# Optimization experiments

Measured on AMD Instinct MI355X. Metric: run time of the kernel, lower is better.

Reference implementation:

```python
import jax, jax.numpy as jnp
import numpy as np

B, S, D, H, L, MLP, WIN = 4, 1024, 256, 8, 2, 1024, 64
HD = D // H
NEG = -1e9  # emulates -inf additive mask; exp underflows to exact 0

_idx = jnp.arange(S)
BAND = jnp.where(jnp.abs(_idx[:, None] - _idx[None, :]) <= WIN, 0.0, NEG).astype(jnp.float32)


def setup_inputs() -> dict:
    key = jax.random.key(0)
    ks = iter(jax.random.split(key, 16))
    r = lambda shape, s=0.02: jax.random.normal(next(ks), shape, dtype=jnp.float32) * s
    return {
        "x": jax.random.normal(next(ks), (B, S, D), dtype=jnp.float32),
        "scale": jnp.ones((1,), jnp.float32) * (D ** -0.5),
        "Win_a": r((L, 3 * D, D)), "bin_a": jnp.zeros((L, 3 * D), jnp.float32),
        "Wout_a": r((L, D, D)), "bout_a": jnp.zeros((L, D), jnp.float32),
        "Win_e": r((L, 3 * D, D)), "bin_e": jnp.zeros((L, 3 * D), jnp.float32),
        "Wout_e": r((L, D, D)), "bout_e": jnp.zeros((L, D), jnp.float32),
        "ln1_g": jnp.ones((L, D), jnp.float32), "ln1_b": jnp.zeros((L, D), jnp.float32),
        "ln2_g": jnp.ones((L, D), jnp.float32), "ln2_b": jnp.zeros((L, D), jnp.float32),
        "W1": r((L, MLP, D)), "b1": jnp.zeros((L, MLP), jnp.float32),
        "W2": r((L, D, MLP)), "b2": jnp.zeros((L, D), jnp.float32),
        "lnf_g": jnp.ones((D,), jnp.float32), "lnf_b": jnp.zeros((D,), jnp.float32),
    }


def _layernorm(x, g, b, eps=1e-5):
    m = jnp.mean(x, axis=-1, keepdims=True)
    v = jnp.mean(jnp.square(x - m), axis=-1, keepdims=True)
    return (x - m) * jax.lax.rsqrt(v + eps) * g + b


def _mha(x, Win, bin_, Wout, bout, mask=None):
    # torch nn.MultiheadAttention (batch_first=True), dropout=0
    b, s, _ = x.shape
    qkv = x @ Win.T + bin_                       # (b, s, 3D)
    q, k, v = jnp.split(qkv, 3, axis=-1)
    split = lambda t: t.reshape(b, s, H, HD).transpose(0, 2, 1, 3)  # (b, H, s, HD)
    q, k, v = split(q), split(k), split(v)
    scores = jnp.einsum('bhqd,bhkd->bhqk', q, k) / np.float32(np.sqrt(HD))
    if mask is not None:
        scores = scores + mask
    attn = jax.nn.softmax(scores, axis=-1)
    out = jnp.einsum('bhqk,bhkd->bhqd', attn, v).transpose(0, 2, 1, 3).reshape(b, s, D)
    return out @ Wout.T + bout


def reference(x, scale, Win_a, bin_a, Wout_a, bout_a, Win_e, bin_e, Wout_e, bout_e,
              ln1_g, ln1_b, ln2_g, ln2_b, W1, b1, W2, b2, lnf_g, lnf_b):
    # ScaledSinusoidalPositionalEncoding returns arange(S)*scale, shape (S,1)
    pos = jnp.arange(S, dtype=jnp.float32) * scale[0]   # (S,)
    x = x + pos[:, None]                                 # broadcast (B,S,D)+(S,1)
    for l in range(L):
        xi = _mha(x, Win_a[l], bin_a[l], Wout_a[l], bout_a[l])
        x = _layernorm(x + xi, ln1_g[l], ln1_b[l])
        xe = _mha(x, Win_e[l], bin_e[l], Wout_e[l], bout_e[l], mask=BAND)
        attended = _layernorm(x + xe, ln2_g[l], ln2_b[l])
        h = jax.nn.gelu(attended @ W1[l].T + b1[l], approximate=False)
        x = attended + h @ W2[l].T + b2[l]
    return _layernorm(x, lnf_g, lnf_b)
```

## Files before the change

kernel.cpp:

```cpp
#include <hip/hip_runtime.h>
#include <math.h>

#define BB 4
#define SS 1024
#define DD 256
#define HH 8
#define HD 32
#define D3 768
#define MLP 1024
#define NTOK (BB * SS)
#define NSEG 4

typedef __attribute__((ext_vector_type(8))) short short8;
typedef __attribute__((ext_vector_type(4))) float f32x4;

__device__ __forceinline__ unsigned short f2bfu(float f) {
    union { float f; unsigned i; } u; u.f = f;
    unsigned r = u.i + 0x7fffu + ((u.i >> 16) & 1u);
    return (unsigned short)(r >> 16);
}
__device__ __forceinline__ float bfu2f(unsigned short h) {
    union { unsigned i; float f; } u; u.i = ((unsigned)h) << 16; return u.f;
}

#define W_TOT 2097152
#define WL0   196608
#define WBLK  (W_TOT / 256)
#define PBLK  (NTOK * DD / 256)
__global__ __launch_bounds__(256) void prep_kernel(
    const float* __restrict__ a0, const float* __restrict__ a1,
    const float* __restrict__ a2, const float* __restrict__ a3,
    const float* __restrict__ a4, const float* __restrict__ a5,
    unsigned short* __restrict__ out, unsigned short* __restrict__ out_lo,
    const float* __restrict__ x, const float* __restrict__ scale,
    float* __restrict__ xf, unsigned short* __restrict__ xh,
    unsigned short* __restrict__ xl)
{
    if (blockIdx.x < WBLK) {
        int i = blockIdx.x * 256 + threadIdx.x;
        const float* s; int off;
        if      (i <  393216) { s = a0; off = 0;       }
        else if (i <  524288) { s = a1; off = 393216;  }
        else if (i <  917504) { s = a2; off = 524288;  }
        else if (i < 1048576) { s = a3; off = 917504;  }
        else if (i < 1572864) { s = a4; off = 1048576; }
        else                  { s = a5; off = 1572864; }
        float v = s[i - off];
        unsigned short h = f2bfu(v);
        out[i] = h;
        if (i < WL0) out_lo[i] = f2bfu(v - bfu2f(h));
    } else {
        int i = (blockIdx.x - WBLK) * 256 + threadIdx.x;
        int s = (i >> 8) & (SS - 1);
        float v = x[i] + (float)s * scale[0];
        xf[i] = v;
        unsigned short h = f2bfu(v);
        xh[i] = h;
        xl[i] = f2bfu(v - bfu2f(h));
    }
}

__device__ __forceinline__ size_t vt_index(int row, int col512) {
    int b = row >> 10, s = row & (SS - 1);
    int h = col512 >> 5, d = col512 & (HD - 1);
    return (((size_t)b * HH + h) * HD + d) * SS + s;
}

#define LDP 40
template<int BN>
__global__ __launch_bounds__(256) void gemm_mfma(
    const unsigned short* __restrict__ A, const unsigned short* __restrict__ W,
    const float* __restrict__ bias, const float* __restrict__ resid,
    float* __restrict__ outf, unsigned short* __restrict__ outb,
    unsigned short* __restrict__ vth,
    int M, int N, int K, int act)
{
    constexpr int NJ = BN / 32;
    __shared__ __align__(16) unsigned short As[64 * LDP];
    __shared__ __align__(16) unsigned short Bs[BN * LDP];
    const int t = threadIdx.x;
    const int lane = t & 63, wave = t >> 6;
    const int wr = wave >> 1, wc = wave & 1;
    const int m0 = blockIdx.y * 64, n0 = blockIdx.x * BN;
    const int sr = t >> 2;
    const int sc = (t & 3) * 8;

    const unsigned short* Ag = A + (size_t)(m0 + sr) * K + sc;
    const unsigned short* Wg = W + (size_t)(n0 + sr) * K + sc;

    f32x4 acc[2][NJ];
    #pragma unroll
    for (int i = 0; i < 2; i++)
        #pragma unroll
        for (int j = 0; j < NJ; j++)
            acc[i][j] = (f32x4){0.f, 0.f, 0.f, 0.f};

    const int lm = lane & 15, lk = (lane >> 4) * 8;

    uint4 a0 = *(const uint4*)(Ag);
    uint4 b0 = *(const uint4*)(Wg);
    uint4 b1;
    if constexpr (BN == 128) b1 = *(const uint4*)(Wg + (size_t)64 * K);

    for (int k0 = 0; k0 < K; k0 += 32) {
        __syncthreads();
        *(uint4*)&As[sr * LDP + sc] = a0;
        *(uint4*)&Bs[sr * LDP + sc] = b0;
        if constexpr (BN == 128) *(uint4*)&Bs[(sr + 64) * LDP + sc] = b1;
        __syncthreads();
        if (k0 + 32 < K) {
            a0 = *(const uint4*)(Ag + k0 + 32);
            b0 = *(const uint4*)(Wg + k0 + 32);
            if constexpr (BN == 128)
                b1 = *(const uint4*)(Wg + (size_t)64 * K + k0 + 32);
        }

        short8 af[2], bf[NJ];
        #pragma unroll
        for (int i = 0; i < 2; i++)
            af[i] = *(const short8*)&As[(wr * 32 + i * 16 + lm) * LDP + lk];
        #pragma unroll
        for (int j = 0; j < NJ; j++)
            bf[j] = *(const short8*)&Bs[(wc * (BN / 2) + j * 16 + lm) * LDP + lk];
        #pragma unroll
        for (int i = 0; i < 2; i++)
            #pragma unroll
            for (int j = 0; j < NJ; j++)
                acc[i][j] = __builtin_amdgcn_mfma_f32_16x16x32_bf16(
                    af[i], bf[j], acc[i][j], 0, 0, 0);
    }

    const int lq = lane >> 4;
    #pragma unroll
    for (int j = 0; j < NJ; j++) {
        int col = n0 + wc * (BN / 2) + j * 16 + lm;
        float bv = bias[col];
        #pragma unroll
        for (int i = 0; i < 2; i++) {
            #pragma unroll
            for (int r = 0; r < 4; r++) {
                int row = m0 + wr * 32 + i * 16 + lq * 4 + r;
                float v = acc[i][j][r] + bv;
                if (act) v = 0.5f * v * (1.0f + erff(v * 0.70710678118654752f));
                if (vth && col >= 2 * DD) {
                    vth[vt_index(row, col - 2 * DD)] = f2bfu(v);
                } else {
                    size_t idx = (size_t)row * N + col;
                    if (resid) v += resid[idx];
                    if (outf) outf[idx] = v;
                    if (outb) outb[idx] = f2bfu(v);
                }
            }
        }
    }
}

template<bool COMBINE, bool DOLN, int K>
__global__ __launch_bounds__(256) void gemm_ln(
    const unsigned short* __restrict__ A,
    const float* __restrict__ Of, const float2* __restrict__ Ml,
    const unsigned short* __restrict__ W, const float* __restrict__ bias,
    const float* __restrict__ resid,
    const float* __restrict__ g, const float* __restrict__ bt,
    float* __restrict__ outf, unsigned short* __restrict__ outb)
{
    constexpr int LDA = K + 8;
    constexpr int NS  = K / 32;
    __shared__ __align__(16) unsigned short As[16 * LDA];
    __shared__ float rsum[4][16];
    __shared__ float rsum2[4][16];
    const int t = threadIdx.x;
    const int lane = t & 63, wave = t >> 6;
    const int m0 = blockIdx.x * 16;
    const int lm = lane & 15, quad = lane >> 4;

    const unsigned short* Wp = W + (size_t)(wave * 64 + lm) * K + quad * 8;
    short8 bf[4][4];
    #pragma unroll
    for (int s = 0; s < 4; s++)
        #pragma unroll
        for (int j = 0; j < 4; j++)
            bf[s][j] = *(const short8*)(Wp + (size_t)(j * 16) * K + s * 32);

    if (COMBINE) {
        const int row = t >> 4, cg = t & 15;
        const int token = m0 + row;
        const int h = cg >> 1;
        float2 ml[NSEG];
        float M = -1e30f;
        #pragma unroll
        for (int s = 0; s < NSEG; s++) {
            ml[s] = Ml[((size_t)s * NTOK + token) * HH + h];
            M = fmaxf(M, ml[s].x);
        }
        float wgt[NSEG]; float denom = 0.f;
        #pragma unroll
        for (int s = 0; s < NSEG; s++) {
            wgt[s] = __expf(ml[s].x - M);
            denom += ml[s].y * wgt[s];
        }
        const float inv = 1.0f / denom;
        float a16[16];
        #pragma unroll
        for (int c = 0; c < 16; c++) a16[c] = 0.f;
        #pragma unroll
        for (int s = 0; s < NSEG; s++) {
            const float* p = Of + ((size_t)s * NTOK + token) * DD + cg * 16;
            #pragma unroll
            for (int c4 = 0; c4 < 4; c4++) {
                float4 x = *(const float4*)(p + c4 * 4);
                a16[c4 * 4 + 0] += x.x * wgt[s];
                a16[c4 * 4 + 1] += x.y * wgt[s];
                a16[c4 * 4 + 2] += x.z * wgt[s];
                a16[c4 * 4 + 3] += x.w * wgt[s];
            }
        }
        __align__(16) unsigned short ab[16];
        #pragma unroll
        for (int c = 0; c < 16; c++) ab[c] = f2bfu(a16[c] * inv);
        *(uint4*)&As[row * LDA + cg * 16]     = *(uint4*)&ab[0];
        *(uint4*)&As[row * LDA + cg * 16 + 8] = *(uint4*)&ab[8];
    } else {
        #pragma unroll
        for (int u = t; u < 16 * (K / 8); u += 256) {
            int row = u / (K / 8), cg = u % (K / 8);
            *(uint4*)&As[row * LDA + cg * 8] =
                *(const uint4*)(A + (size_t)(m0 + row) * K + cg * 8);
        }
    }
    __syncthreads();

    f32x4 acc[4];
    #pragma unroll
    for (int j = 0; j < 4; j++) acc[j] = (f32x4){0.f, 0.f, 0.f, 0.f};

    #pragma unroll
    for (int k = 0; k < NS; k++) {
        const int r4 = k & 3;
        short8 af = *(const short8*)&As[lm * LDA + k * 32 + quad * 8];
        #pragma unroll
        for (int j = 0; j < 4; j++)
            acc[j] = __builtin_amdgcn_mfma_f32_16x16x32_bf16(
                af, bf[r4][j], acc[j], 0, 0, 0);
        if (k + 4 < NS) {
            #pragma unroll
            for (int j = 0; j < 4; j++)
                bf[r4][j] = *(const short8*)(Wp + (size_t)(j * 16) * K
                                             + (k + 4) * 32);
        }
    }

    #pragma unroll
    for (int j = 0; j < 4; j++) {
        int col = wave * 64 + j * 16 + lm;
        float bv = bias[col];
        #pragma unroll
        for (int r = 0; r < 4; r++) {
            int row = m0 + quad * 4 + r;
            acc[j][r] += bv + resid[(size_t)row * DD + col];
        }
    }
    if (!DOLN) {
        #pragma unroll
        for (int j = 0; j < 4; j++) {
            int col = wave * 64 + j * 16 + lm;
            #pragma unroll
            for (int r = 0; r < 4; r++) {
                int row = m0 + quad * 4 + r;
                size_t idx = (size_t)row * DD + col;
                if (outf) outf[idx] = acc[j][r];
                if (outb) outb[idx] = f2bfu(acc[j][r]);
            }
        }
        return;
    }
    #pragma unroll
    for (int r = 0; r < 4; r++) {
        float s = 0.f;
        #pragma unroll
        for (int j = 0; j < 4; j++) s += acc[j][r];
        s += __shfl_xor(s, 1, 64); s += __shfl_xor(s, 2, 64);
        s += __shfl_xor(s, 4, 64); s += __shfl_xor(s, 8, 64);
        if (lm == 0) rsum[wave][quad * 4 + r] = s;
    }
    __syncthreads();
    float mean_[4];
    #pragma unroll
    for (int r = 0; r < 4; r++) {
        int ri = quad * 4 + r;
        mean_[r] = (rsum[0][ri] + rsum[1][ri] + rsum[2][ri] + rsum[3][ri])
                 * (1.0f / 256.0f);
    }
    #pragma unroll
    for (int r = 0; r < 4; r++) {
        float s2 = 0.f;
        #pragma unroll
        for (int j = 0; j < 4; j++) {
            float d = acc[j][r] - mean_[r];
            s2 += d * d;
        }
        s2 += __shfl_xor(s2, 1, 64); s2 += __shfl_xor(s2, 2, 64);
        s2 += __shfl_xor(s2, 4, 64); s2 += __shfl_xor(s2, 8, 64);
        if (lm == 0) rsum2[wave][quad * 4 + r] = s2;
    }
    __syncthreads();
    float rstd[4];
    #pragma unroll
    for (int r = 0; r < 4; r++) {
        int ri = quad * 4 + r;
        rstd[r] = rsqrtf((rsum2[0][ri] + rsum2[1][ri] + rsum2[2][ri] + rsum2[3][ri])
                         * (1.0f / 256.0f) + 1e-5f);
    }
    #pragma unroll
    for (int j = 0; j < 4; j++) {
        int col = wave * 64 + j * 16 + lm;
        float gv = g[col], bv2 = bt[col];
        #pragma unroll
        for (int r = 0; r < 4; r++) {
            int row = m0 + quad * 4 + r;
            float ov = (acc[j][r] - mean_[r]) * rstd[r] * gv + bv2;
            size_t idx = (size_t)row * DD + col;
            if (outf) outf[idx] = ov;
            if (outb) outb[idx] = f2bfu(ov);
        }
    }
}

__global__ __launch_bounds__(256) void gemm_mfma_split(
    const unsigned short* __restrict__ Ah, const unsigned short* __restrict__ Al,
    const unsigned short* __restrict__ Wh, const unsigned short* __restrict__ Wl,
    const float* __restrict__ bias,
    unsigned short* __restrict__ outh, unsigned short* __restrict__ outl,
    unsigned short* __restrict__ vth,
    int M, int N, int K)
{
    __shared__ __align__(16) unsigned short Ash[64 * LDP];
    __shared__ __align__(16) unsigned short Asl[64 * LDP];
    __shared__ __align__(16) unsigned short Bsh[64 * LDP];
    __shared__ __align__(16) unsigned short Bsl[64 * LDP];
    const int t = threadIdx.x;
    const int lane = t & 63, wave = t >> 6;
    const int wr = wave >> 1, wc = wave & 1;
    const int m0 = blockIdx.y * 64, n0 = blockIdx.x * 64;
    const int sr = t >> 2;
    const int sc = (t & 3) * 8;

    const size_t oA = (size_t)(m0 + sr) * K + sc;
    const size_t oW = (size_t)(n0 + sr) * K + sc;

    f32x4 acc[2][2];
    #pragma unroll
    for (int i = 0; i < 2; i++)
        #pragma unroll
        for (int j = 0; j < 2; j++)
            acc[i][j] = (f32x4){0.f, 0.f, 0.f, 0.f};

    const int lm = lane & 15, lk = (lane >> 4) * 8;

    uint4 ah0 = *(const uint4*)(Ah + oA);
    uint4 al0 = *(const uint4*)(Al + oA);
    uint4 bh0 = *(const uint4*)(Wh + oW);
    uint4 bl0 = *(const uint4*)(Wl + oW);

    for (int k0 = 0; k0 < K; k0 += 32) {
        __syncthreads();
        *(uint4*)&Ash[sr * LDP + sc] = ah0;
        *(uint4*)&Asl[sr * LDP + sc] = al0;
        *(uint4*)&Bsh[sr * LDP + sc] = bh0;
        *(uint4*)&Bsl[sr * LDP + sc] = bl0;
        __syncthreads();
        if (k0 + 32 < K) {
            ah0 = *(const uint4*)(Ah + oA + k0 + 32);
            al0 = *(const uint4*)(Al + oA + k0 + 32);
            bh0 = *(const uint4*)(Wh + oW + k0 + 32);
            bl0 = *(const uint4*)(Wl + oW + k0 + 32);
        }

        short8 afh[2], afl[2], bfh[2], bfl[2];
        #pragma unroll
        for (int i = 0; i < 2; i++) {
            afh[i] = *(const short8*)&Ash[(wr * 32 + i * 16 + lm) * LDP + lk];
            afl[i] = *(const short8*)&Asl[(wr * 32 + i * 16 + lm) * LDP + lk];
        }
        #pragma unroll
        for (int j = 0; j < 2; j++) {
            bfh[j] = *(const short8*)&Bsh[(wc * 32 + j * 16 + lm) * LDP + lk];
            bfl[j] = *(const short8*)&Bsl[(wc * 32 + j * 16 + lm) * LDP + lk];
        }
        #pragma unroll
        for (int i = 0; i < 2; i++)
            #pragma unroll
            for (int j = 0; j < 2; j++) {
                acc[i][j] = __builtin_amdgcn_mfma_f32_16x16x32_bf16(
                    afl[i], bfh[j], acc[i][j], 0, 0, 0);
                acc[i][j] = __builtin_amdgcn_mfma_f32_16x16x32_bf16(
                    afh[i], bfl[j], acc[i][j], 0, 0, 0);
                acc[i][j] = __builtin_amdgcn_mfma_f32_16x16x32_bf16(
                    afh[i], bfh[j], acc[i][j], 0, 0, 0);
            }
    }

    const int lq = lane >> 4;
    #pragma unroll
    for (int j = 0; j < 2; j++) {
        int col = n0 + wc * 32 + j * 16 + lm;
        float bv = bias[col];
        #pragma unroll
        for (int i = 0; i < 2; i++) {
            #pragma unroll
            for (int r = 0; r < 4; r++) {
                int row = m0 + wr * 32 + i * 16 + lq * 4 + r;
                float v = acc[i][j][r] + bv;
                unsigned short h = f2bfu(v);
                if (col >= 2 * DD) {
                    vth[vt_index(row, col - 2 * DD)] = h;
                } else {
                    size_t idx = (size_t)row * N + col;
                    outh[idx] = h;
                    outl[idx] = f2bfu(v - bfu2f(h));
                }
            }
        }
    }
}

__global__ __launch_bounds__(256) void attn_split(
    const unsigned short* __restrict__ qkvh,
    const unsigned short* __restrict__ qkvl,
    const unsigned short* __restrict__ vth,
    float* __restrict__ Of, float2* __restrict__ Ml)
{
    __shared__ __align__(16) unsigned short Ks [64 * 40];
    __shared__ __align__(16) unsigned short Vt [32 * 72];
    __shared__ __align__(16) unsigned short Ps [64 * 72];
    __shared__ __align__(16) unsigned short Ksl[64 * 40];

    const int t = threadIdx.x;
    const int wave = t >> 6, lane = t & 63;
    const int lm = lane & 15, quad = lane >> 4;
    const int i0 = blockIdx.x * 64, h = blockIdx.y;
    const int z = blockIdx.z;
    const int b = z >> 2, seg = z & (NSEG - 1);
    const int sr = t >> 2, sc8 = (t & 3) * 8;
    const int vd = t >> 3, vs8 = (t & 7) * 8;

    const size_t qoff = ((size_t)(b * SS) + i0 + 16 * wave + lm) * D3 + h * HD + quad * 8;
    short8 qh = *(const short8*)(qkvh + qoff);
    short8 ql = *(const short8*)(qkvl + qoff);

    const unsigned short* Kg  = qkvh + (size_t)(b * SS) * D3 + DD + h * HD;
    const unsigned short* Klg = qkvl + (size_t)(b * SS) * D3 + DD + h * HD;
    const unsigned short* Vg  = vth + ((size_t)b * HH + h) * HD * SS;

    float m = -1e30f, l = 0.f;
    f32x4 o[2];
    o[0] = (f32x4){0.f, 0.f, 0.f, 0.f};
    o[1] = (f32x4){0.f, 0.f, 0.f, 0.f};

    const int per = (SS / 64) / NSEG;
    const int s0 = seg * per, s1 = s0 + per - 1;
    const float scl = 0.17677669529663688f;

    short8 kreg  = *(const short8*)(Kg  + (size_t)(s0 * 64 + sr) * D3 + sc8);
    short8 kregl = *(const short8*)(Klg + (size_t)(s0 * 64 + sr) * D3 + sc8);
    short8 vreg  = *(const short8*)(Vg  + (size_t)vd * SS + s0 * 64 + vs8);

    for (int kt = s0; kt <= s1; kt++) {
        const int k0 = kt * 64;
        __syncthreads();
        *(short8*)&Ks [sr * 40 + sc8] = kreg;
        *(short8*)&Ksl[sr * 40 + sc8] = kregl;
        *(short8*)&Vt [vd * 72 + vs8] = vreg;
        __syncthreads();
        if (kt < s1) {
            kreg  = *(const short8*)(Kg  + (size_t)(k0 + 64 + sr) * D3 + sc8);
            kregl = *(const short8*)(Klg + (size_t)(k0 + 64 + sr) * D3 + sc8);
            vreg  = *(const short8*)(Vg  + (size_t)vd * SS + k0 + 64 + vs8);
        }

        float vs[4][4];
        #pragma unroll
        for (int cb = 0; cb < 4; cb++) {
            short8 kf  = *(const short8*)&Ks [(16 * cb + lm) * 40 + quad * 8];
            short8 kfl = *(const short8*)&Ksl[(16 * cb + lm) * 40 + quad * 8];
            f32x4 a = (f32x4){0.f, 0.f, 0.f, 0.f};
            a = __builtin_amdgcn_mfma_f32_16x16x32_bf16(kf,  ql, a, 0, 0, 0);
            a = __builtin_amdgcn_mfma_f32_16x16x32_bf16(kfl, qh, a, 0, 0, 0);
            a = __builtin_amdgcn_mfma_f32_16x16x32_bf16(kf,  qh, a, 0, 0, 0);
            #pragma unroll
            for (int r = 0; r < 4; r++) vs[cb][r] = a[r] * scl;
        }

        float tm = fmaxf(fmaxf(vs[0][0], vs[0][1]), fmaxf(vs[0][2], vs[0][3]));
        #pragma unroll
        for (int cb = 1; cb < 4; cb++)
            tm = fmaxf(tm, fmaxf(fmaxf(vs[cb][0], vs[cb][1]),
                                 fmaxf(vs[cb][2], vs[cb][3])));
        tm = fmaxf(tm, __shfl_xor(tm, 16, 64));
        tm = fmaxf(tm, __shfl_xor(tm, 32, 64));
        float mn = fmaxf(m, tm);
        float alpha = __expf(m - mn);
        m = mn;

        float ps = 0.f;
        #pragma unroll
        for (int cb = 0; cb < 4; cb++) {
            float p0 = __expf(vs[cb][0] - mn), p1 = __expf(vs[cb][1] - mn);
            float p2 = __expf(vs[cb][2] - mn), p3 = __expf(vs[cb][3] - mn);
            ps += (p0 + p1) + (p2 + p3);
            uint2 pk;
            pk.x = (unsigned)f2bfu(p0) | ((unsigned)f2bfu(p1) << 16);
            pk.y = (unsigned)f2bfu(p2) | ((unsigned)f2bfu(p3) << 16);
            *(uint2*)&Ps[(16 * wave + lm) * 72 + 16 * cb + quad * 4] = pk;
        }
        ps += __shfl_xor(ps, 16, 64);
        ps += __shfl_xor(ps, 32, 64);
        l = l * alpha + ps;

        float ar[4];
        #pragma unroll
        for (int r = 0; r < 4; r++) ar[r] = __shfl(alpha, quad * 4 + r, 64);
        #pragma unroll
        for (int r = 0; r < 4; r++) { o[0][r] *= ar[r]; o[1][r] *= ar[r]; }

        #pragma unroll
        for (int kc = 0; kc < 2; kc++) {
            short8 pf = *(const short8*)&Ps[(16 * wave + lm) * 72 + 32 * kc + quad * 8];
            #pragma unroll
            for (int nh = 0; nh < 2; nh++) {
                short8 vf = *(const short8*)&Vt[(16 * nh + lm) * 72 + 32 * kc + quad * 8];
                o[nh] = __builtin_amdgcn_mfma_f32_16x16x32_bf16(pf, vf, o[nh], 0, 0, 0);
            }
        }
    }

    #pragma unroll
    for (int r = 0; r < 4; r++) {
        int row = i0 + 16 * wave + quad * 4 + r;
        size_t base = ((size_t)seg * NTOK + b * SS + row) * DD + h * HD + lm;
        Of[base]      = o[0][r];
        Of[base + 16] = o[1][r];
    }
    if (quad == 0)
        Ml[((size_t)seg * NTOK + b * SS + i0 + 16 * wave + lm) * HH + h] =
            make_float2(m, l);
}

__global__ __launch_bounds__(256) void attn_fixed(
    const unsigned short* __restrict__ qkvh,
    const unsigned short* __restrict__ vth,
    unsigned short* __restrict__ outb,
    float* __restrict__ Of, float2* __restrict__ Ml,
    int win, int nseg)
{
    __shared__ __align__(16) unsigned short Ks[64 * 40];
    __shared__ __align__(16) unsigned short Vt[32 * 72];
    __shared__ __align__(16) unsigned short Ps[64 * 72];

    const int t = threadIdx.x;
    const int wave = t >> 6, lane = t & 63;
    const int lm = lane & 15, quad = lane >> 4;
    const int i0 = blockIdx.x * 64, h = blockIdx.y;
    const int z = blockIdx.z;
    const int b = z / nseg, seg = z - b * nseg;
    const int sr = t >> 2, sc8 = (t & 3) * 8;
    const int vd = t >> 3, vs8 = (t & 7) * 8;

    const size_t qoff = ((size_t)(b * SS) + i0 + 16 * wave + lm) * D3 + h * HD + quad * 8;
    short8 qh = *(const short8*)(qkvh + qoff);

    const unsigned short* Kg = qkvh + (size_t)(b * SS) * D3 + DD + h * HD;
    const unsigned short* Vg = vth + ((size_t)b * HH + h) * HD * SS;

    float l = 0.f;
    f32x4 o[2];
    o[0] = (f32x4){0.f, 0.f, 0.f, 0.f};
    o[1] = (f32x4){0.f, 0.f, 0.f, 0.f};

    int t0 = 0, t1 = SS / 64 - 1;
    const bool masked = (win < SS);
    if (masked) {
        t0 = (i0 - win) >> 6;        if (t0 < 0) t0 = 0;
        t1 = (i0 + 63 + win) >> 6;   if (t1 > SS / 64 - 1) t1 = SS / 64 - 1;
    }
    const int per = (t1 - t0 + nseg) / nseg;
    const int s0 = t0 + seg * per;
    const int s1 = (s0 + per - 1 < t1) ? (s0 + per - 1) : t1;
    const float scl = 0.17677669529663688f;
    const float M0 = 32.0f;

    const int qrow = i0 + 16 * wave + lm;

    short8 kreg = *(const short8*)(Kg + (size_t)(s0 * 64 + sr) * D3 + sc8);
    short8 vreg = *(const short8*)(Vg + (size_t)vd * SS + s0 * 64 + vs8);

    for (int kt = s0; kt <= s1; kt++) {
        const int k0 = kt * 64;
        __syncthreads();
        *(short8*)&Ks[sr * 40 + sc8] = kreg;
        *(short8*)&Vt[vd * 72 + vs8] = vreg;
        __syncthreads();
        if (kt < s1) {
            kreg = *(const short8*)(Kg + (size_t)(k0 + 64 + sr) * D3 + sc8);
            vreg = *(const short8*)(Vg + (size_t)vd * SS + k0 + 64 + vs8);
        }

        #pragma unroll
        for (int cb = 0; cb < 4; cb++) {
            short8 kf = *(const short8*)&Ks[(16 * cb + lm) * 40 + quad * 8];
            f32x4 a = (f32x4){0.f, 0.f, 0.f, 0.f};
            a = __builtin_amdgcn_mfma_f32_16x16x32_bf16(kf, qh, a, 0, 0, 0);
            float p[4];
            #pragma unroll
            for (int r = 0; r < 4; r++) {
                float v = a[r] * scl;
                if (masked) {
                    int di = qrow - (k0 + 16 * cb + quad * 4 + r);
                    if (di > win || di < -win) v = -1e30f;
                }
                p[r] = __expf(v - M0);
            }
            l += (p[0] + p[1]) + (p[2] + p[3]);
            uint2 pk;
            pk.x = (unsigned)f2bfu(p[0]) | ((unsigned)f2bfu(p[1]) << 16);
            pk.y = (unsigned)f2bfu(p[2]) | ((unsigned)f2bfu(p[3]) << 16);
            *(uint2*)&Ps[(16 * wave + lm) * 72 + 16 * cb + quad * 4] = pk;
        }

        #pragma unroll
        for (int kc = 0; kc < 2; kc++) {
            short8 pf = *(const short8*)&Ps[(16 * wave + lm) * 72 + 32 * kc + quad * 8];
            #pragma unroll
            for (int nh = 0; nh < 2; nh++) {
                short8 vf = *(const short8*)&Vt[(16 * nh + lm) * 72 + 32 * kc + quad * 8];
                o[nh] = __builtin_amdgcn_mfma_f32_16x16x32_bf16(pf, vf, o[nh], 0, 0, 0);
            }
        }
    }

    l += __shfl_xor(l, 16, 64);
    l += __shfl_xor(l, 32, 64);

    if (nseg == 1) {
        #pragma unroll
        for (int r = 0; r < 4; r++) {
            float lr = __shfl(l, quad * 4 + r, 64);
            float invl = 1.0f / lr;
            size_t base = ((size_t)(b * SS) + i0 + 16 * wave + quad * 4 + r) * DD + h * HD + lm;
            outb[base]      = f2bfu(o[0][r] * invl);
            outb[base + 16] = f2bfu(o[1][r] * invl);
        }
    } else {
        #pragma unroll
        for (int r = 0; r < 4; r++) {
            int row = i0 + 16 * wave + quad * 4 + r;
            size_t base = ((size_t)seg * NTOK + b * SS + row) * DD + h * HD + lm;
            Of[base]      = o[0][r];
            Of[base + 16] = o[1][r];
        }
        if (quad == 0)
            Ml[((size_t)seg * NTOK + b * SS + i0 + 16 * wave + lm) * HH + h] =
                make_float2(M0, l);
    }
}

extern "C" void kernel_launch(void* const* d_in, const int* in_sizes, int n_in,
                              void* d_out, int out_size, void* d_ws, size_t ws_size,
                              hipStream_t stream)
{
    const float* xin   = (const float*)d_in[0];
    const float* scale = (const float*)d_in[1];
    const float* Win_a = (const float*)d_in[2];
    const float* bin_a = (const float*)d_in[3];
    const float* Wout_a= (const float*)d_in[4];
    const float* bout_a= (const float*)d_in[5];
    const float* Win_e = (const float*)d_in[6];
    const float* bin_e = (const float*)d_in[7];
    const float* Wout_e= (const float*)d_in[8];
    const float* bout_e= (const float*)d_in[9];
    const float* ln1_g = (const float*)d_in[10];
    const float* ln1_b = (const float*)d_in[11];
    const float* ln2_g = (const float*)d_in[12];
    const float* ln2_b = (const float*)d_in[13];
    const float* W1    = (const float*)d_in[14];
    const float* b1    = (const float*)d_in[15];
    const float* W2    = (const float*)d_in[16];
    const float* b2    = (const float*)d_in[17];
    const float* lnf_g = (const float*)d_in[18];
    const float* lnf_b = (const float*)d_in[19];

    char* ws = (char*)d_ws;
    float* X    = (float*)ws;                     ws += (size_t)NTOK * DD * 4;
    float* X2   = (float*)ws;                     ws += (size_t)NTOK * DD * 4;
    unsigned short* Xb   = (unsigned short*)ws;   ws += (size_t)NTOK * DD * 2;
    unsigned short* Xlb  = (unsigned short*)ws;   ws += (size_t)NTOK * DD * 2;
    unsigned short* X2b  = (unsigned short*)ws;   ws += (size_t)NTOK * DD * 2;
    unsigned short* ATb  = (unsigned short*)ws;   ws += (size_t)NTOK * DD * 2;
    unsigned short* QKVb = (unsigned short*)ws;   ws += (size_t)NTOK * D3 * 2;
    unsigned short* QKVl = (unsigned short*)ws;   ws += (size_t)NTOK * D3 * 2;
    unsigned short* VTh  = (unsigned short*)ws;   ws += (size_t)NTOK * DD * 2;
    unsigned short* HMLb = (unsigned short*)ws;   ws += (size_t)NTOK * MLP * 2;
    unsigned short* Wb   = (unsigned short*)ws;   ws += (size_t)W_TOT * 2;
    unsigned short* Wl0  = (unsigned short*)ws;   ws += (size_t)WL0 * 2;
    float2* Ml           = (float2*)ws;           ws += (size_t)NSEG * NTOK * HH * 8;
    float* Of            = (float*)ws;            ws += (size_t)NSEG * NTOK * DD * 4;

    unsigned short* WinA_b  = Wb + 0;
    unsigned short* WoutA_b = Wb + 393216;
    unsigned short* WinE_b  = Wb + 524288;
    unsigned short* WoutE_b = Wb + 917504;
    unsigned short* W1_b    = Wb + 1048576;
    unsigned short* W2_b    = Wb + 1572864;

    prep_kernel<<<WBLK + PBLK, 256, 0, stream>>>(
        Win_a, Wout_a, Win_e, Wout_e, W1, W2, Wb, Wl0,
        xin, scale, X, Xb, Xlb);

    float* cur = X;            float* oth = X2;
    unsigned short* curb = Xb; unsigned short* othb = X2b;

    for (int l = 0; l < 2; l++) {
        if (l == 0) {
            gemm_mfma_split<<<dim3(D3 / 64, NTOK / 64), 256, 0, stream>>>(
                Xb, Xlb, WinA_b, Wl0, bin_a, QKVb, QKVl, VTh, NTOK, D3, DD);
            attn_split<<<dim3(SS / 64, HH, BB * NSEG), 256, 0, stream>>>(
                QKVb, QKVl, VTh, Of, Ml);
        } else {
            gemm_mfma<64><<<dim3(D3 / 64, NTOK / 64), 256, 0, stream>>>(
                curb, WinA_b + (size_t)l * D3 * DD, bin_a + (size_t)l * D3,
                nullptr, nullptr, QKVb, VTh, NTOK, D3, DD, 0);
            attn_fixed<<<dim3(SS / 64, HH, BB * NSEG), 256, 0, stream>>>(
                QKVb, VTh, nullptr, Of, Ml, 1 << 28, NSEG);
        }
        gemm_ln<true, true, DD><<<NTOK / 16, 256, 0, stream>>>(
            nullptr, Of, Ml, WoutA_b + (size_t)l * DD * DD,
            bout_a + (size_t)l * DD, cur,
            ln1_g + l * DD, ln1_b + l * DD, oth, othb);

        gemm_mfma<64><<<dim3(D3 / 64, NTOK / 64), 256, 0, stream>>>(
            othb, WinE_b + (size_t)l * D3 * DD, bin_e + (size_t)l * D3,
            nullptr, nullptr, QKVb, VTh, NTOK, D3, DD, 0);
        attn_fixed<<<dim3(SS / 64, HH, BB), 256, 0, stream>>>(
            QKVb, VTh, ATb, nullptr, nullptr, 64, 1);
        gemm_ln<false, true, DD><<<NTOK / 16, 256, 0, stream>>>(
            ATb, nullptr, nullptr, WoutE_b + (size_t)l * DD * DD,
            bout_e + (size_t)l * DD, oth,
            ln2_g + l * DD, ln2_b + l * DD, cur, curb);

        gemm_mfma<128><<<dim3(MLP / 128, NTOK / 64), 256, 0, stream>>>(
            curb, W1_b + (size_t)l * MLP * DD, b1 + (size_t)l * MLP,
            nullptr, nullptr, HMLb, nullptr, NTOK, MLP, DD, 1);
        if (l == 0) {
            gemm_ln<false, false, MLP><<<NTOK / 16, 256, 0, stream>>>(
                HMLb, nullptr, nullptr, W2_b + (size_t)l * DD * MLP,
                b2 + (size_t)l * DD, cur,
                nullptr, nullptr, oth, othb);
            float* tf = cur; cur = oth; oth = tf;
            unsigned short* tb = curb; curb = othb; othb = tb;
        } else {
            gemm_ln<false, true, MLP><<<NTOK / 16, 256, 0, stream>>>(
                HMLb, nullptr, nullptr, W2_b + (size_t)l * DD * MLP,
                b2 + (size_t)l * DD, cur,
                lnf_g, lnf_b, (float*)d_out, nullptr);
        }
    }
}
```

Measured before the change: 300.6 us.

## Drop split-KV segmentation for full attention, normalize output directly in attention kernel

```diff
diff --git a/kernel.cpp b/kernel.cpp
--- a/kernel.cpp
+++ b/kernel.cpp
@@ -155,10 +155,9 @@
     }
 }
 
-template<bool COMBINE, bool DOLN, int K>
+template<bool DOLN, int K>
 __global__ __launch_bounds__(256) void gemm_ln(
     const unsigned short* __restrict__ A,
-    const float* __restrict__ Of, const float2* __restrict__ Ml,
     const unsigned short* __restrict__ W, const float* __restrict__ bias,
     const float* __restrict__ resid,
     const float* __restrict__ g, const float* __restrict__ bt,
@@ -182,51 +181,11 @@
         for (int j = 0; j < 4; j++)
             bf[s][j] = *(const short8*)(Wp + (size_t)(j * 16) * K + s * 32);
 
-    if (COMBINE) {
-        const int row = t >> 4, cg = t & 15;
-        const int token = m0 + row;
-        const int h = cg >> 1;
-        float2 ml[NSEG];
-        float M = -1e30f;
-        #pragma unroll
-        for (int s = 0; s < NSEG; s++) {
-            ml[s] = Ml[((size_t)s * NTOK + token) * HH + h];
-            M = fmaxf(M, ml[s].x);
-        }
-        float wgt[NSEG]; float denom = 0.f;
-        #pragma unroll
-        for (int s = 0; s < NSEG; s++) {
-            wgt[s] = __expf(ml[s].x - M);
-            denom += ml[s].y * wgt[s];
-        }
-        const float inv = 1.0f / denom;
-        float a16[16];
-        #pragma unroll
-        for (int c = 0; c < 16; c++) a16[c] = 0.f;
-        #pragma unroll
-        for (int s = 0; s < NSEG; s++) {
-            const float* p = Of + ((size_t)s * NTOK + token) * DD + cg * 16;
-            #pragma unroll
-            for (int c4 = 0; c4 < 4; c4++) {
-                float4 x = *(const float4*)(p + c4 * 4);
-                a16[c4 * 4 + 0] += x.x * wgt[s];
-                a16[c4 * 4 + 1] += x.y * wgt[s];
-                a16[c4 * 4 + 2] += x.z * wgt[s];
-                a16[c4 * 4 + 3] += x.w * wgt[s];
-            }
-        }
-        __align__(16) unsigned short ab[16];
-        #pragma unroll
-        for (int c = 0; c < 16; c++) ab[c] = f2bfu(a16[c] * inv);
-        *(uint4*)&As[row * LDA + cg * 16]     = *(uint4*)&ab[0];
-        *(uint4*)&As[row * LDA + cg * 16 + 8] = *(uint4*)&ab[8];
-    } else {
-        #pragma unroll
-        for (int u = t; u < 16 * (K / 8); u += 256) {
-            int row = u / (K / 8), cg = u % (K / 8);
-            *(uint4*)&As[row * LDA + cg * 8] =
-                *(const uint4*)(A + (size_t)(m0 + row) * K + cg * 8);
-        }
+    #pragma unroll
+    for (int u = t; u < 16 * (K / 8); u += 256) {
+        int row = u / (K / 8), cg = u % (K / 8);
+        *(uint4*)&As[row * LDA + cg * 8] =
+            *(const uint4*)(A + (size_t)(m0 + row) * K + cg * 8);
     }
     __syncthreads();
 
@@ -428,7 +387,7 @@
     const unsigned short* __restrict__ qkvh,
     const unsigned short* __restrict__ qkvl,
     const unsigned short* __restrict__ vth,
-    float* __restrict__ Of, float2* __restrict__ Ml)
+    unsigned short* __restrict__ outb)
 {
     __shared__ __align__(16) unsigned short Ks [64 * 40];
     __shared__ __align__(16) unsigned short Vt [32 * 72];
@@ -439,8 +398,7 @@
     const int wave = t >> 6, lane = t & 63;
     const int lm = lane & 15, quad = lane >> 4;
     const int i0 = blockIdx.x * 64, h = blockIdx.y;
-    const int z = blockIdx.z;
-    const int b = z >> 2, seg = z & (NSEG - 1);
+    const int b = blockIdx.z;
     const int sr = t >> 2, sc8 = (t & 3) * 8;
     const int vd = t >> 3, vs8 = (t & 7) * 8;
 
@@ -457,15 +415,14 @@
     o[0] = (f32x4){0.f, 0.f, 0.f, 0.f};
     o[1] = (f32x4){0.f, 0.f, 0.f, 0.f};
 
-    const int per = (SS / 64) / NSEG;
-    const int s0 = seg * per, s1 = s0 + per - 1;
+    const int s1 = SS / 64 - 1;
     const float scl = 0.17677669529663688f;
 
-    short8 kreg  = *(const short8*)(Kg  + (size_t)(s0 * 64 + sr) * D3 + sc8);
-    short8 kregl = *(const short8*)(Klg + (size_t)(s0 * 64 + sr) * D3 + sc8);
-    short8 vreg  = *(const short8*)(Vg  + (size_t)vd * SS + s0 * 64 + vs8);
-
-    for (int kt = s0; kt <= s1; kt++) {
+    short8 kreg  = *(const short8*)(Kg  + (size_t)sr * D3 + sc8);
+    short8 kregl = *(const short8*)(Klg + (size_t)sr * D3 + sc8);
+    short8 vreg  = *(const short8*)(Vg  + (size_t)vd * SS + vs8);
+
+    for (int kt = 0; kt <= s1; kt++) {
         const int k0 = kt * 64;
         __syncthreads();
         *(short8*)&Ks [sr * 40 + sc8] = kreg;
@@ -536,14 +493,12 @@
 
     #pragma unroll
     for (int r = 0; r < 4; r++) {
-        int row = i0 + 16 * wave + quad * 4 + r;
-        size_t base = ((size_t)seg * NTOK + b * SS + row) * DD + h * HD + lm;
-        Of[base]      = o[0][r];
-        Of[base + 16] = o[1][r];
-    }
-    if (quad == 0)
-        Ml[((size_t)seg * NTOK + b * SS + i0 + 16 * wave + lm) * HH + h] =
-            make_float2(m, l);
+        float lr = __shfl(l, quad * 4 + r, 64);
+        float invl = 1.0f / lr;
+        size_t base = ((size_t)(b * SS) + i0 + 16 * wave + quad * 4 + r) * DD + h * HD + lm;
+        outb[base]      = f2bfu(o[0][r] * invl);
+        outb[base + 16] = f2bfu(o[1][r] * invl);
+    }
 }
 
 __global__ __launch_bounds__(256) void attn_fixed(
@@ -704,6 +659,7 @@
     unsigned short* Wl0  = (unsigned short*)ws;   ws += (size_t)WL0 * 2;
     float2* Ml           = (float2*)ws;           ws += (size_t)NSEG * NTOK * HH * 8;
     float* Of            = (float*)ws;            ws += (size_t)NSEG * NTOK * DD * 4;
+    (void)Ml; (void)Of;
 
     unsigned short* WinA_b  = Wb + 0;
     unsigned short* WoutA_b = Wb + 393216;
@@ -723,17 +679,17 @@
         if (l == 0) {
             gemm_mfma_split<<<dim3(D3 / 64, NTOK / 64), 256, 0, stream>>>(
                 Xb, Xlb, WinA_b, Wl0, bin_a, QKVb, QKVl, VTh, NTOK, D3, DD);
-            attn_split<<<dim3(SS / 64, HH, BB * NSEG), 256, 0, stream>>>(
-                QKVb, QKVl, VTh, Of, Ml);
+            attn_split<<<dim3(SS / 64, HH, BB), 256, 0, stream>>>(
+                QKVb, QKVl, VTh, ATb);
         } else {
             gemm_mfma<64><<<dim3(D3 / 64, NTOK / 64), 256, 0, stream>>>(
                 curb, WinA_b + (size_t)l * D3 * DD, bin_a + (size_t)l * D3,
                 nullptr, nullptr, QKVb, VTh, NTOK, D3, DD, 0);
-            attn_fixed<<<dim3(SS / 64, HH, BB * NSEG), 256, 0, stream>>>(
-                QKVb, VTh, nullptr, Of, Ml, 1 << 28, NSEG);
-        }
-        gemm_ln<true, true, DD><<<NTOK / 16, 256, 0, stream>>>(
-            nullptr, Of, Ml, WoutA_b + (size_t)l * DD * DD,
+            attn_fixed<<<dim3(SS / 64, HH, BB), 256, 0, stream>>>(
+                QKVb, VTh, ATb, nullptr, nullptr, 1 << 28, 1);
+        }
+        gemm_ln<true, DD><<<NTOK / 16, 256, 0, stream>>>(
+            ATb, WoutA_b + (size_t)l * DD * DD,
             bout_a + (size_t)l * DD, cur,
             ln1_g + l * DD, ln1_b + l * DD, oth, othb);
 
@@ -742,8 +698,8 @@
             nullptr, nullptr, QKVb, VTh, NTOK, D3, DD, 0);
         attn_fixed<<<dim3(SS / 64, HH, BB), 256, 0, stream>>>(
             QKVb, VTh, ATb, nullptr, nullptr, 64, 1);
-        gemm_ln<false, true, DD><<<NTOK / 16, 256, 0, stream>>>(
-            ATb, nullptr, nullptr, WoutE_b + (size_t)l * DD * DD,
+        gemm_ln<true, DD><<<NTOK / 16, 256, 0, stream>>>(
+            ATb, WoutE_b + (size_t)l * DD * DD,
             bout_e + (size_t)l * DD, oth,
             ln2_g + l * DD, ln2_b + l * DD, cur, curb);
 
@@ -751,15 +707,15 @@
             curb, W1_b + (size_t)l * MLP * DD, b1 + (size_t)l * MLP,
             nullptr, nullptr, HMLb, nullptr, NTOK, MLP, DD, 1);
         if (l == 0) {
-            gemm_ln<false, false, MLP><<<NTOK / 16, 256, 0, stream>>>(
-                HMLb, nullptr, nullptr, W2_b + (size_t)l * DD * MLP,
+            gemm_ln<false, MLP><<<NTOK / 16, 256, 0, stream>>>(
+                HMLb, W2_b + (size_t)l * DD * MLP,
                 b2 + (size_t)l * DD, cur,
                 nullptr, nullptr, oth, othb);
             float* tf = cur; cur = oth; oth = tf;
             unsigned short* tb = curb; curb = othb; othb = tb;
         } else {
-            gemm_ln<false, true, MLP><<<NTOK / 16, 256, 0, stream>>>(
-                HMLb, nullptr, nullptr, W2_b + (size_t)l * DD * MLP,
+            gemm_ln<true, MLP><<<NTOK / 16, 256, 0, stream>>>(
+                HMLb, W2_b + (size_t)l * DD * MLP,
                 b2 + (size_t)l * DD, cur,
                 lnf_g, lnf_b, (float*)d_out, nullptr);
         }
```

After: 304.0 us. Within noise of the previous version (+1.1%).
